# Performance work log

Measured on AMD Instinct MI355X. Metric: run time of the kernel, lower is better.

The kernel has to match this reference:

```python
import jax, jax.numpy as jnp
import numpy as np

N_NODES = 50000
K_CHEB = 3


def _norm_weights(edge_index, num_nodes):
    # PyG ChebConv with normalization='sym', lambda_max=2.0:
    # L_hat = (2/lambda_max) * (I - D^-1/2 A D^-1/2) - I = -D^-1/2 A D^-1/2
    src, dst = edge_index[0], edge_index[1]
    ones = jnp.ones(src.shape[0], dtype=jnp.float32)
    deg = jax.ops.segment_sum(ones, src, num_segments=num_nodes)
    dis = jnp.where(deg > 0, jax.lax.rsqrt(jnp.maximum(deg, 1.0)), 0.0)
    w = dis[src] * dis[dst]  # [E]
    return src, dst, w


def _cheb_conv(x, src, dst, w, W, b, num_nodes):
    # W: [K, in, out], b: [out]
    def lap(v):  # L_hat @ v = -(D^-1/2 A D^-1/2) v via gather + segment-sum
        return -jax.ops.segment_sum(w[:, None] * v[src], dst, num_segments=num_nodes)
    Tx0 = x
    out = Tx0 @ W[0]
    Tx1 = lap(x)
    out = out + Tx1 @ W[1]
    for k in range(2, W.shape[0]):
        Tx2 = 2.0 * lap(Tx1) - Tx0
        out = out + Tx2 @ W[k]
        Tx0, Tx1 = Tx1, Tx2
    return out + b


def setup_inputs() -> dict:
    key = jax.random.key(0)
    ks = jax.random.split(key, 9)
    N, E, F_IN, F_HID, F_OUT = N_NODES, 800000, 128, 64, 16
    x = jax.random.normal(ks[0], (N, F_IN), dtype=jnp.float32)
    edge_index = jax.random.randint(ks[1], (2, E), 0, N, dtype=jnp.int64)
    def glorot(k, kk, fi, fo):
        s = (6.0 / (fi + fo)) ** 0.5
        return jax.random.uniform(k, (kk, fi, fo), jnp.float32, -s, s)
    W1 = glorot(ks[2], K_CHEB, F_IN, F_HID)
    b1 = jnp.zeros((F_HID,), jnp.float32)
    Wm = glorot(ks[3], K_CHEB, F_HID, F_HID)
    bm = jnp.zeros((F_HID,), jnp.float32)
    W2 = glorot(ks[4], K_CHEB, F_HID, F_OUT)
    b2 = jnp.zeros((F_OUT,), jnp.float32)
    return {"x": x, "edge_index": edge_index, "W1": W1, "b1": b1,
            "Wm": Wm, "bm": bm, "W2": W2, "b2": b2}


def reference(x, edge_index, W1, b1, Wm, bm, W2, b2):
    src, dst, w = _norm_weights(edge_index, N_NODES)
    h = jax.nn.relu(_cheb_conv(x, src, dst, w, W1, b1, N_NODES))
    # dropout is identity in eval mode (training=False)
    h = jax.nn.relu(_cheb_conv(h, src, dst, w, Wm, bm, N_NODES))
    out = _cheb_conv(h, src, dst, w, W2, b2, N_NODES)
    return out
```

## Files before the change

kernel.cpp:

```cpp
#include <hip/hip_runtime.h>
#include <hip/hip_fp16.h>

constexpr int NNODES = 50000;
constexpr int NS  = 64;
constexpr int NR  = 4;
constexpr int RSZ = 12500;

typedef _Float16 half8_t __attribute__((ext_vector_type(8)));
typedef _Float16 half4_t __attribute__((ext_vector_type(4)));
typedef float    f32x4_t __attribute__((ext_vector_type(4)));

template<int CH> struct hvec_sel;
template<> struct hvec_sel<4> { using T = half4_t; };
template<> struct hvec_sel<8> { using T = half8_t; };


template<int FIN, int FOUT>
__device__ void pack_dev(const float* __restrict__ W, _Float16* __restrict__ Bp,
                         int b, int nb) {
  constexpr int NT = 3 * FOUT / 16;
  constexpr int KT = FIN / 32;
  const int total = KT * NT * 512;
  for (int i = b * 256 + (int)threadIdx.x; i < total; i += nb * 256) {
    int j = i & 7;
    int lane = (i >> 3) & 63;
    int tile = i >> 9;
    int nt = tile % NT, kt = tile / NT;
    int k = kt * 32 + (lane >> 4) * 8 + j;
    int n = nt * 16 + (lane & 15);
    int cheb = n / FOUT, c = n - cheb * FOUT;
    Bp[i] = (_Float16)W[((size_t)cheb * FIN + k) * FOUT + c];
  }
}

template<int FIN, int FOUT, typename IN_T>
__device__ void gemm_dev(const IN_T* __restrict__ X, const _Float16* __restrict__ Bp,
                         const float* __restrict__ b, _Float16* __restrict__ A,
                         _Float16* __restrict__ U, _Float16* __restrict__ V,
                         int N, int blk, _Float16* xs) {
  constexpr int NT = 3 * FOUT / 16;
  constexpr int C3 = NT / 3;
  constexpr int KT = FIN / 32;
  constexpr int LDR = FIN + 8;

  const int tid = threadIdx.x;
  const int row0 = blk * 64;

  for (int i = tid * 4; i < 64 * FIN; i += 1024) {
    int r = i / FIN, k = i - r * FIN;
    int row = row0 + r;
    short4 hv = make_short4(0, 0, 0, 0);
    if (row < N) {
      if constexpr (sizeof(IN_T) == 4) {
        float4 v = *(const float4*)((const float*)X + (size_t)row * FIN + k);
        _Float16 h0 = (_Float16)v.x, h1 = (_Float16)v.y, h2 = (_Float16)v.z, h3 = (_Float16)v.w;
        hv = make_short4(*(short*)&h0, *(short*)&h1, *(short*)&h2, *(short*)&h3);
      } else {
        hv = *(const short4*)((const _Float16*)X + (size_t)row * FIN + k);
      }
    }
    *(short4*)(&xs[r * LDR + k]) = hv;
  }
  __syncthreads();

  const int wave = tid >> 6, lane = tid & 63;
  const int m = lane & 15, quad = lane >> 4;

  f32x4_t acc[NT];
  #pragma unroll
  for (int nt = 0; nt < NT; ++nt) acc[nt] = (f32x4_t){0.f, 0.f, 0.f, 0.f};

  #pragma unroll
  for (int kt = 0; kt < KT; ++kt) {
    half8_t a = *(const half8_t*)(&xs[(wave * 16 + m) * LDR + kt * 32 + quad * 8]);
    const half8_t* bp = (const half8_t*)Bp + (size_t)(kt * NT) * 64 + lane;
    #pragma unroll
    for (int nt = 0; nt < NT; ++nt) {
      half8_t bf = bp[(size_t)nt * 64];
      acc[nt] = __builtin_amdgcn_mfma_f32_16x16x32_f16(a, bf, acc[nt], 0, 0, 0);
    }
  }

  const int row_b = row0 + wave * 16 + quad * 4;
  #pragma unroll
  for (int nt = 0; nt < C3; ++nt) {
    int c = nt * 16 + m;
    float bb = b[c];
    #pragma unroll
    for (int r = 0; r < 4; ++r) {
      int row = row_b + r;
      if (row < N) {
        size_t o = (size_t)row * FOUT + c;
        A[o] = (_Float16)(acc[nt][r] - acc[nt + 2 * C3][r] + bb);
        U[o] = (_Float16)acc[nt + C3][r];
        V[o] = (_Float16)acc[nt + 2 * C3][r];
      }
    }
  }
}


__global__ void __launch_bounds__(256) k1_hist_pack(const int* __restrict__ ei, int E, int ES,
    int* __restrict__ part_src, int* __restrict__ part_dst,
    const float* __restrict__ W1, const float* __restrict__ Wm, const float* __restrict__ W2,
    _Float16* __restrict__ Bp1, _Float16* __restrict__ Bp2, _Float16* __restrict__ Bp3) {
  __shared__ int sh[RSZ];
  const int bid = blockIdx.x;
  if (bid < 512) {
    const int z = bid & 1, r = (bid >> 1) & 3, s = bid >> 3;
    for (int i = threadIdx.x; i < RSZ; i += 256) sh[i] = 0;
    __syncthreads();
    const int lo = r * RSZ;
    const int* __restrict__ idxarr = ei + (z ? E : 0);
    const int e0 = s * ES, e1 = min(e0 + ES, E);
    for (int e = e0 + (int)threadIdx.x; e < e1; e += 256) {
      unsigned u = (unsigned)(idxarr[e] - lo);
      if (u < (unsigned)RSZ) atomicAdd(&sh[u], 1);
    }
    __syncthreads();
    int* __restrict__ part = z ? part_dst : part_src;
    const int base = (s * NR + r) * RSZ;
    for (int i = threadIdx.x; i < RSZ; i += 256) part[base + i] = sh[i];
  } else if (bid < 536) {
    pack_dev<128, 64>(W1, Bp1, bid - 512, 24);
  } else if (bid < 548) {
    pack_dev<64, 64>(Wm, Bp2, bid - 536, 12);
  } else {
    pack_dev<64, 16>(W2, Bp3, bid - 548, 3);
  }
}


__global__ void __launch_bounds__(256) k2_reduce_scan(const int* __restrict__ part_src,
    int* __restrict__ part_dst, float* __restrict__ dis, int* __restrict__ cnt,
    int* __restrict__ exc, int* __restrict__ bsum, int N) {
  __shared__ int sh[256];
  const int tid = threadIdx.x;
  const int n = blockIdx.x * 256 + tid;
  int off = 0;
  if (n < N) {
    int r = n / RSZ, i = n - r * RSZ;
    int ssum = 0;
    #pragma unroll 4
    for (int s = 0; s < NS; ++s) ssum += part_src[(size_t)(s * NR + r) * RSZ + i];
    dis[n] = (ssum > 0) ? rsqrtf((float)ssum) : 0.0f;
    for (int s = 0; s < NS; ++s) {
      size_t idx = (size_t)(s * NR + r) * RSZ + i;
      int c = part_dst[idx];
      part_dst[idx] = off;
      off += c;
    }
    cnt[n] = off;
  }
  int acc = off;
  sh[tid] = acc; __syncthreads();
  #pragma unroll
  for (int o = 1; o < 256; o <<= 1) {
    int t = (tid >= o) ? sh[tid - o] : 0;
    __syncthreads();
    acc += t;
    sh[tid] = acc;
    __syncthreads();
  }
  if (n < N) exc[n] = acc - off;
  if (tid == 255) bsum[blockIdx.x] = acc;
}


__global__ void __launch_bounds__(256) k2b_scan2(int* __restrict__ bsum, int NB) {
  __shared__ int sh[256];
  int tid = threadIdx.x;
  int v = (tid < NB) ? bsum[tid] : 0;
  int acc = v;
  sh[tid] = acc; __syncthreads();
  #pragma unroll
  for (int o = 1; o < 256; o <<= 1) {
    int t = (tid >= o) ? sh[tid - o] : 0;
    __syncthreads();
    acc += t;
    sh[tid] = acc;
    __syncthreads();
  }
  if (tid < NB) bsum[tid] = acc - v;
}


__global__ void __launch_bounds__(256) k3_fill_gemm1(const int* __restrict__ ei, int E, int ES,
    const int* __restrict__ exc, const int* __restrict__ bsumx,
    const int* __restrict__ pd_off, const float* __restrict__ dis, int2* __restrict__ ew,
    const float* __restrict__ x, const _Float16* __restrict__ Bp1, const float* __restrict__ b1,
    _Float16* __restrict__ Ah, _Float16* __restrict__ Uh, _Float16* __restrict__ Vh, int N) {
  __shared__ __align__(16) char smem[50048];
  const int bid = blockIdx.x;
  if (bid < 256) {
    int* cur = (int*)smem;
    for (int i = threadIdx.x; i < RSZ; i += 256) cur[i] = 0;
    __syncthreads();
    const int s = bid >> 2, r = bid & 3;
    const int lo = r * RSZ;
    const int base = (s * NR + r) * RSZ;
    const int e0 = s * ES, e1 = min(e0 + ES, E);
    for (int e = e0 + (int)threadIdx.x; e < e1; e += 256) {
      int sv = ei[e], d = ei[E + e];
      unsigned u = (unsigned)(d - lo);
      if (u < (unsigned)RSZ) {
        int rank = atomicAdd(&cur[u], 1);
        int pos = exc[d] + bsumx[d >> 8] + pd_off[base + u] + rank;
        float w = -dis[sv] * dis[d];
        ew[pos] = make_int2(sv, __float_as_int(w));
      }
    }
  } else {
    gemm_dev<128, 64, float>(x, Bp1, b1, Ah, Uh, Vh, N, bid - 256, (_Float16*)smem);
  }
}


template<int FIN, int FOUT>
__global__ void __launch_bounds__(256) gemm_mfma_kernel(const _Float16* __restrict__ X,
    const _Float16* __restrict__ Bp, const float* __restrict__ b,
    _Float16* __restrict__ A, _Float16* __restrict__ U, _Float16* __restrict__ V, int N) {
  __shared__ _Float16 xs[64 * (FIN + 8)];
  gemm_dev<FIN, FOUT, _Float16>(X, Bp, b, A, U, V, N, blockIdx.x, xs);
}


template<int F, int CH>
__global__ void __launch_bounds__(256) lapA_kernel(const void* __restrict__ Vp,
    const void* __restrict__ Up, void* __restrict__ Yp,
    const int* __restrict__ exc, const int* __restrict__ cnt, const int* __restrict__ bsumx,
    const int2* __restrict__ ew, int N) {
  using HT = typename hvec_sel<CH>::T;
  constexpr int H = F / CH;
  const HT* __restrict__ Vv = (const HT*)Vp;
  int t = blockIdx.x * 256 + threadIdx.x;
  int n = t / H;
  if (n >= N) return;
  int h = t - n * H;
  int j = exc[n] + bsumx[n >> 8];
  int e = j + cnt[n];
  float acc[CH];
  #pragma unroll
  for (int i = 0; i < CH; ++i) acc[i] = 0.f;
  for (; j + 7 < e; j += 8) {
    int2 c[8]; HT v[8];
    #pragma unroll
    for (int q = 0; q < 8; ++q) c[q] = ew[j + q];
    #pragma unroll
    for (int q = 0; q < 8; ++q) v[q] = Vv[(size_t)c[q].x * H + h];
    #pragma unroll
    for (int q = 0; q < 8; ++q) {
      float w = __int_as_float(c[q].y);
      #pragma unroll
      for (int i = 0; i < CH; ++i) acc[i] = fmaf(w, (float)v[q][i], acc[i]);
    }
  }
  for (; j + 3 < e; j += 4) {
    int2 c[4]; HT v[4];
    #pragma unroll
    for (int q = 0; q < 4; ++q) c[q] = ew[j + q];
    #pragma unroll
    for (int q = 0; q < 4; ++q) v[q] = Vv[(size_t)c[q].x * H + h];
    #pragma unroll
    for (int q = 0; q < 4; ++q) {
      float w = __int_as_float(c[q].y);
      #pragma unroll
      for (int i = 0; i < CH; ++i) acc[i] = fmaf(w, (float)v[q][i], acc[i]);
    }
  }
  for (; j < e; ++j) {
    int2 c = ew[j];
    float w = __int_as_float(c.y);
    HT v = Vv[(size_t)c.x * H + h];
    #pragma unroll
    for (int i = 0; i < CH; ++i) acc[i] = fmaf(w, (float)v[i], acc[i]);
  }
  HT u = ((const HT*)Up)[t];
  HT y;
  #pragma unroll
  for (int i = 0; i < CH; ++i) y[i] = (_Float16)fmaf(2.f, acc[i], (float)u[i]);
  ((HT*)Yp)[t] = y;
}

template<int F, int CH, bool RELU, bool OUT32>
__global__ void __launch_bounds__(256) lapB_kernel(const void* __restrict__ Yp,
    const void* __restrict__ Ap,
    const int* __restrict__ exc, const int* __restrict__ cnt, const int* __restrict__ bsumx,
    const int2* __restrict__ ew, void* __restrict__ outp, int N) {
  using HT = typename hvec_sel<CH>::T;
  constexpr int H = F / CH;
  const HT* __restrict__ Yv = (const HT*)Yp;
  int t = blockIdx.x * 256 + threadIdx.x;
  int n = t / H;
  if (n >= N) return;
  int h = t - n * H;
  int j = exc[n] + bsumx[n >> 8];
  int e = j + cnt[n];
  float acc[CH];
  #pragma unroll
  for (int i = 0; i < CH; ++i) acc[i] = 0.f;
  for (; j + 7 < e; j += 8) {
    int2 c[8]; HT v[8];
    #pragma unroll
    for (int q = 0; q < 8; ++q) c[q] = ew[j + q];
    #pragma unroll
    for (int q = 0; q < 8; ++q) v[q] = Yv[(size_t)c[q].x * H + h];
    #pragma unroll
    for (int q = 0; q < 8; ++q) {
      float w = __int_as_float(c[q].y);
      #pragma unroll
      for (int i = 0; i < CH; ++i) acc[i] = fmaf(w, (float)v[q][i], acc[i]);
    }
  }
  for (; j + 3 < e; j += 4) {
    int2 c[4]; HT v[4];
    #pragma unroll
    for (int q = 0; q < 4; ++q) c[q] = ew[j + q];
    #pragma unroll
    for (int q = 0; q < 4; ++q) v[q] = Yv[(size_t)c[q].x * H + h];
    #pragma unroll
    for (int q = 0; q < 4; ++q) {
      float w = __int_as_float(c[q].y);
      #pragma unroll
      for (int i = 0; i < CH; ++i) acc[i] = fmaf(w, (float)v[q][i], acc[i]);
    }
  }
  for (; j < e; ++j) {
    int2 c = ew[j];
    float w = __int_as_float(c.y);
    HT v = Yv[(size_t)c.x * H + h];
    #pragma unroll
    for (int i = 0; i < CH; ++i) acc[i] = fmaf(w, (float)v[i], acc[i]);
  }
  HT a = ((const HT*)Ap)[t];
  float r[CH];
  #pragma unroll
  for (int i = 0; i < CH; ++i) {
    r[i] = (float)a[i] + acc[i];
    if (RELU) r[i] = fmaxf(r[i], 0.f);
  }
  if constexpr (OUT32) {
    float4* o4 = (float4*)outp;
    #pragma unroll
    for (int q = 0; q < CH / 4; ++q)
      o4[(size_t)t * (CH / 4) + q] = make_float4(r[4 * q], r[4 * q + 1], r[4 * q + 2], r[4 * q + 3]);
  } else {
    HT y;
    #pragma unroll
    for (int i = 0; i < CH; ++i) y[i] = (_Float16)r[i];
    ((HT*)outp)[t] = y;
  }
}


extern "C" void kernel_launch(void* const* d_in, const int* in_sizes, int n_in,
                              void* d_out, int out_size, void* d_ws, size_t ws_size,
                              hipStream_t stream) {
  const float* x  = (const float*)d_in[0];
  const int*   ei = (const int*)d_in[1];
  const float* W1 = (const float*)d_in[2];
  const float* b1 = (const float*)d_in[3];
  const float* Wm = (const float*)d_in[4];
  const float* bm = (const float*)d_in[5];
  const float* W2 = (const float*)d_in[6];
  const float* b2 = (const float*)d_in[7];
  float* out = (float*)d_out;
  const int N = NNODES;
  const int E = in_sizes[1] / 2;
  const int ES = (E + NS - 1) / NS;
  const int NB = (N + 255) / 256;

  char* p = (char*)d_ws;
  auto alloc = [&](size_t bytes) -> char* {
    char* q = p;
    p += (bytes + 255) & ~(size_t)255;
    return q;
  };
  int*      part_src = (int*)alloc((size_t)NS * NR * RSZ * 4);
  int*      part_dst = (int*)alloc((size_t)NS * NR * RSZ * 4);
  int*      cnt      = (int*)alloc((size_t)N * 4);
  int*      exc      = (int*)alloc((size_t)N * 4);
  int*      bsum     = (int*)alloc(1024);
  float*    dis      = (float*)alloc((size_t)N * 4);
  int2*     ew       = (int2*)alloc((size_t)E * 8);
  _Float16* Xh       = (_Float16*)alloc((size_t)N * 64 * 2);
  _Float16* Ah       = (_Float16*)alloc((size_t)N * 64 * 2);
  _Float16* Uh       = (_Float16*)alloc((size_t)N * 64 * 2);
  _Float16* Vh       = (_Float16*)alloc((size_t)N * 64 * 2);
  _Float16* Yh       = (_Float16*)alloc((size_t)N * 64 * 2);
  _Float16* Bp1      = (_Float16*)alloc((size_t)128 * 192 * 2);
  _Float16* Bp2      = (_Float16*)alloc((size_t)64 * 192 * 2);
  _Float16* Bp3      = (_Float16*)alloc((size_t)64 * 48 * 2);

  k1_hist_pack<<<551, 256, 0, stream>>>(ei, E, ES, part_src, part_dst,
                                        W1, Wm, W2, Bp1, Bp2, Bp3);
  k2_reduce_scan<<<NB, 256, 0, stream>>>(part_src, part_dst, dis, cnt, exc, bsum, N);
  k2b_scan2<<<1, 256, 0, stream>>>(bsum, NB);
  k3_fill_gemm1<<<256 + 782, 256, 0, stream>>>(ei, E, ES, exc, bsum, part_dst, dis, ew,
                                               x, Bp1, b1, Ah, Uh, Vh, N);

  const int gmm  = (N + 63) / 64;
  const int g64c = (N * 8 + 255) / 256;
  const int g16c = (N * 4 + 255) / 256;

  lapA_kernel<64, 8><<<g64c, 256, 0, stream>>>(Vh, Uh, Yh, exc, cnt, bsum, ew, N);
  lapB_kernel<64, 8, true, false><<<g64c, 256, 0, stream>>>(Yh, Ah, exc, cnt, bsum, ew, Xh, N);

  gemm_mfma_kernel<64, 64><<<gmm, 256, 0, stream>>>(Xh, Bp2, bm, Ah, Uh, Vh, N);
  lapA_kernel<64, 8><<<g64c, 256, 0, stream>>>(Vh, Uh, Yh, exc, cnt, bsum, ew, N);
  lapB_kernel<64, 8, true, false><<<g64c, 256, 0, stream>>>(Yh, Ah, exc, cnt, bsum, ew, Xh, N);

  gemm_mfma_kernel<64, 16><<<gmm, 256, 0, stream>>>(Xh, Bp3, b2, Ah, Uh, Vh, N);
  lapA_kernel<16, 4><<<g16c, 256, 0, stream>>>(Vh, Uh, Yh, exc, cnt, bsum, ew, N);
  lapB_kernel<16, 4, false, true><<<g16c, 256, 0, stream>>>(Yh, Ah, exc, cnt, bsum, ew, out, N);
}
```

Measured before the change: 269.4 us.

## Compress edge list to 32-bit packed src+fp16 weight and factor dst scaling

Packs each CSR edge into 32 bits: a 16-bit source index and the fp16 source-side normalisation. The destination-side dis factor moves out of the per-edge weight and is applied once per node in the Laplacian epilogues. Histogram partials shrink to u16 with an s*N layout, and per-edge ranks are recorded during the histogram so the fill pass no longer needs shared-memory atomics. The aim is to cut edge-stream bandwidth in all six SpMM passes and the cost of the preprocessing. In exchange it relies on N < 65536 and per-slice degree < 256, and lowers weight precision to fp16.

```diff
diff --git a/kernel.cpp b/kernel.cpp
--- a/kernel.cpp
+++ b/kernel.cpp
@@ -13,6 +13,11 @@
 template<int CH> struct hvec_sel;
 template<> struct hvec_sel<4> { using T = half4_t; };
 template<> struct hvec_sel<8> { using T = half8_t; };
+
+__device__ __forceinline__ float w_of(unsigned ec) {
+  unsigned short wb = (unsigned short)(ec >> 16);
+  return (float)__builtin_bit_cast(_Float16, wb);
+}
 
 
 template<int FIN, int FOUT>
@@ -101,9 +106,11 @@
 
 
 __global__ void __launch_bounds__(256) k1_hist_pack(const int* __restrict__ ei, int E, int ES,
-    int* __restrict__ part_src, int* __restrict__ part_dst,
+    unsigned short* __restrict__ part_src, unsigned short* __restrict__ part_dst,
+    unsigned char* __restrict__ rank,
     const float* __restrict__ W1, const float* __restrict__ Wm, const float* __restrict__ W2,
-    _Float16* __restrict__ Bp1, _Float16* __restrict__ Bp2, _Float16* __restrict__ Bp3) {
+    _Float16* __restrict__ Bp1, _Float16* __restrict__ Bp2, _Float16* __restrict__ Bp3,
+    int N) {
   __shared__ int sh[RSZ];
   const int bid = blockIdx.x;
   if (bid < 512) {
@@ -113,14 +120,25 @@
     const int lo = r * RSZ;
     const int* __restrict__ idxarr = ei + (z ? E : 0);
     const int e0 = s * ES, e1 = min(e0 + ES, E);
-    for (int e = e0 + (int)threadIdx.x; e < e1; e += 256) {
-      unsigned u = (unsigned)(idxarr[e] - lo);
-      if (u < (unsigned)RSZ) atomicAdd(&sh[u], 1);
-    }
-    __syncthreads();
-    int* __restrict__ part = z ? part_dst : part_src;
-    const int base = (s * NR + r) * RSZ;
-    for (int i = threadIdx.x; i < RSZ; i += 256) part[base + i] = sh[i];
+    if (z) {
+      for (int e = e0 + (int)threadIdx.x; e < e1; e += 256) {
+        unsigned u = (unsigned)(idxarr[e] - lo);
+        if (u < (unsigned)RSZ) {
+          int rk = atomicAdd(&sh[u], 1);
+          rank[e] = (unsigned char)rk;
+        }
+      }
+    } else {
+      for (int e = e0 + (int)threadIdx.x; e < e1; e += 256) {
+        unsigned u = (unsigned)(idxarr[e] - lo);
+        if (u < (unsigned)RSZ) atomicAdd(&sh[u], 1);
+      }
+    }
+    __syncthreads();
+    unsigned short* __restrict__ part = z ? part_dst : part_src;
+    const size_t base = (size_t)s * N + lo;
+    for (int i = threadIdx.x; i < RSZ && lo + i < N; i += 256)
+      part[base + i] = (unsigned short)sh[i];
   } else if (bid < 536) {
     pack_dev<128, 64>(W1, Bp1, bid - 512, 24);
   } else if (bid < 548) {
@@ -131,23 +149,22 @@
 }
 
 
-__global__ void __launch_bounds__(256) k2_reduce_scan(const int* __restrict__ part_src,
-    int* __restrict__ part_dst, float* __restrict__ dis, int* __restrict__ cnt,
+__global__ void __launch_bounds__(256) k2_reduce_scan(const unsigned short* __restrict__ part_src,
+    unsigned short* __restrict__ part_dst, _Float16* __restrict__ dis, int* __restrict__ cnt,
     int* __restrict__ exc, int* __restrict__ bsum, int N) {
   __shared__ int sh[256];
   const int tid = threadIdx.x;
   const int n = blockIdx.x * 256 + tid;
   int off = 0;
   if (n < N) {
-    int r = n / RSZ, i = n - r * RSZ;
     int ssum = 0;
     #pragma unroll 4
-    for (int s = 0; s < NS; ++s) ssum += part_src[(size_t)(s * NR + r) * RSZ + i];
-    dis[n] = (ssum > 0) ? rsqrtf((float)ssum) : 0.0f;
+    for (int s = 0; s < NS; ++s) ssum += part_src[(size_t)s * N + n];
+    dis[n] = (_Float16)((ssum > 0) ? rsqrtf((float)ssum) : 0.0f);
     for (int s = 0; s < NS; ++s) {
-      size_t idx = (size_t)(s * NR + r) * RSZ + i;
+      size_t idx = (size_t)s * N + n;
       int c = part_dst[idx];
-      part_dst[idx] = off;
+      part_dst[idx] = (unsigned short)off;
       off += c;
     }
     cnt[n] = off;
@@ -187,31 +204,22 @@
 
 __global__ void __launch_bounds__(256) k3_fill_gemm1(const int* __restrict__ ei, int E, int ES,
     const int* __restrict__ exc, const int* __restrict__ bsumx,
-    const int* __restrict__ pd_off, const float* __restrict__ dis, int2* __restrict__ ew,
+    const unsigned short* __restrict__ pd_off, const unsigned char* __restrict__ rank,
+    const unsigned short* __restrict__ dis_u, unsigned* __restrict__ ew,
     const float* __restrict__ x, const _Float16* __restrict__ Bp1, const float* __restrict__ b1,
     _Float16* __restrict__ Ah, _Float16* __restrict__ Uh, _Float16* __restrict__ Vh, int N) {
-  __shared__ __align__(16) char smem[50048];
+  __shared__ _Float16 xs[64 * (128 + 8)];
   const int bid = blockIdx.x;
   if (bid < 256) {
-    int* cur = (int*)smem;
-    for (int i = threadIdx.x; i < RSZ; i += 256) cur[i] = 0;
-    __syncthreads();
-    const int s = bid >> 2, r = bid & 3;
-    const int lo = r * RSZ;
-    const int base = (s * NR + r) * RSZ;
-    const int e0 = s * ES, e1 = min(e0 + ES, E);
-    for (int e = e0 + (int)threadIdx.x; e < e1; e += 256) {
+    for (int e = bid * 256 + (int)threadIdx.x; e < E; e += 256 * 256) {
       int sv = ei[e], d = ei[E + e];
-      unsigned u = (unsigned)(d - lo);
-      if (u < (unsigned)RSZ) {
-        int rank = atomicAdd(&cur[u], 1);
-        int pos = exc[d] + bsumx[d >> 8] + pd_off[base + u] + rank;
-        float w = -dis[sv] * dis[d];
-        ew[pos] = make_int2(sv, __float_as_int(w));
-      }
+      int s = e / ES;
+      int pos = exc[d] + bsumx[d >> 8] + (int)pd_off[(size_t)s * N + d] + (int)rank[e];
+      unsigned w16 = dis_u[sv];
+      ew[pos] = (unsigned)sv | (w16 << 16);
     }
   } else {
-    gemm_dev<128, 64, float>(x, Bp1, b1, Ah, Uh, Vh, N, bid - 256, (_Float16*)smem);
+    gemm_dev<128, 64, float>(x, Bp1, b1, Ah, Uh, Vh, N, bid - 256, xs);
   }
 }
 
@@ -229,7 +237,7 @@
 __global__ void __launch_bounds__(256) lapA_kernel(const void* __restrict__ Vp,
     const void* __restrict__ Up, void* __restrict__ Yp,
     const int* __restrict__ exc, const int* __restrict__ cnt, const int* __restrict__ bsumx,
-    const int2* __restrict__ ew, int N) {
+    const unsigned* __restrict__ ew, const _Float16* __restrict__ dis, int N) {
   using HT = typename hvec_sel<CH>::T;
   constexpr int H = F / CH;
   const HT* __restrict__ Vv = (const HT*)Vp;
@@ -243,42 +251,43 @@
   #pragma unroll
   for (int i = 0; i < CH; ++i) acc[i] = 0.f;
   for (; j + 7 < e; j += 8) {
-    int2 c[8]; HT v[8];
+    unsigned c[8]; HT v[8];
     #pragma unroll
     for (int q = 0; q < 8; ++q) c[q] = ew[j + q];
     #pragma unroll
-    for (int q = 0; q < 8; ++q) v[q] = Vv[(size_t)c[q].x * H + h];
+    for (int q = 0; q < 8; ++q) v[q] = Vv[(size_t)(c[q] & 0xFFFF) * H + h];
     #pragma unroll
     for (int q = 0; q < 8; ++q) {
-      float w = __int_as_float(c[q].y);
+      float w = w_of(c[q]);
       #pragma unroll
       for (int i = 0; i < CH; ++i) acc[i] = fmaf(w, (float)v[q][i], acc[i]);
     }
   }
   for (; j + 3 < e; j += 4) {
-    int2 c[4]; HT v[4];
+    unsigned c[4]; HT v[4];
     #pragma unroll
     for (int q = 0; q < 4; ++q) c[q] = ew[j + q];
     #pragma unroll
-    for (int q = 0; q < 4; ++q) v[q] = Vv[(size_t)c[q].x * H + h];
+    for (int q = 0; q < 4; ++q) v[q] = Vv[(size_t)(c[q] & 0xFFFF) * H + h];
     #pragma unroll
     for (int q = 0; q < 4; ++q) {
-      float w = __int_as_float(c[q].y);
+      float w = w_of(c[q]);
       #pragma unroll
       for (int i = 0; i < CH; ++i) acc[i] = fmaf(w, (float)v[q][i], acc[i]);
     }
   }
   for (; j < e; ++j) {
-    int2 c = ew[j];
-    float w = __int_as_float(c.y);
-    HT v = Vv[(size_t)c.x * H + h];
+    unsigned c = ew[j];
+    float w = w_of(c);
+    HT v = Vv[(size_t)(c & 0xFFFF) * H + h];
     #pragma unroll
     for (int i = 0; i < CH; ++i) acc[i] = fmaf(w, (float)v[i], acc[i]);
   }
+  float s2 = -2.f * (float)dis[n];
   HT u = ((const HT*)Up)[t];
   HT y;
   #pragma unroll
-  for (int i = 0; i < CH; ++i) y[i] = (_Float16)fmaf(2.f, acc[i], (float)u[i]);
+  for (int i = 0; i < CH; ++i) y[i] = (_Float16)fmaf(s2, acc[i], (float)u[i]);
   ((HT*)Yp)[t] = y;
 }
 
@@ -286,7 +295,8 @@
 __global__ void __launch_bounds__(256) lapB_kernel(const void* __restrict__ Yp,
     const void* __restrict__ Ap,
     const int* __restrict__ exc, const int* __restrict__ cnt, const int* __restrict__ bsumx,
-    const int2* __restrict__ ew, void* __restrict__ outp, int N) {
+    const unsigned* __restrict__ ew, const _Float16* __restrict__ dis,
+    void* __restrict__ outp, int N) {
   using HT = typename hvec_sel<CH>::T;
   constexpr int H = F / CH;
   const HT* __restrict__ Yv = (const HT*)Yp;
@@ -300,43 +310,44 @@
   #pragma unroll
   for (int i = 0; i < CH; ++i) acc[i] = 0.f;
   for (; j + 7 < e; j += 8) {
-    int2 c[8]; HT v[8];
+    unsigned c[8]; HT v[8];
     #pragma unroll
     for (int q = 0; q < 8; ++q) c[q] = ew[j + q];
     #pragma unroll
-    for (int q = 0; q < 8; ++q) v[q] = Yv[(size_t)c[q].x * H + h];
+    for (int q = 0; q < 8; ++q) v[q] = Yv[(size_t)(c[q] & 0xFFFF) * H + h];
     #pragma unroll
     for (int q = 0; q < 8; ++q) {
-      float w = __int_as_float(c[q].y);
+      float w = w_of(c[q]);
       #pragma unroll
       for (int i = 0; i < CH; ++i) acc[i] = fmaf(w, (float)v[q][i], acc[i]);
     }
   }
   for (; j + 3 < e; j += 4) {
-    int2 c[4]; HT v[4];
+    unsigned c[4]; HT v[4];
     #pragma unroll
     for (int q = 0; q < 4; ++q) c[q] = ew[j + q];
     #pragma unroll
-    for (int q = 0; q < 4; ++q) v[q] = Yv[(size_t)c[q].x * H + h];
+    for (int q = 0; q < 4; ++q) v[q] = Yv[(size_t)(c[q] & 0xFFFF) * H + h];
     #pragma unroll
     for (int q = 0; q < 4; ++q) {
-      float w = __int_as_float(c[q].y);
+      float w = w_of(c[q]);
       #pragma unroll
       for (int i = 0; i < CH; ++i) acc[i] = fmaf(w, (float)v[q][i], acc[i]);
     }
   }
   for (; j < e; ++j) {
-    int2 c = ew[j];
-    float w = __int_as_float(c.y);
-    HT v = Yv[(size_t)c.x * H + h];
+    unsigned c = ew[j];
+    float w = w_of(c);
+    HT v = Yv[(size_t)(c & 0xFFFF) * H + h];
     #pragma unroll
     for (int i = 0; i < CH; ++i) acc[i] = fmaf(w, (float)v[i], acc[i]);
   }
+  float s1 = -(float)dis[n];
   HT a = ((const HT*)Ap)[t];
   float r[CH];
   #pragma unroll
   for (int i = 0; i < CH; ++i) {
-    r[i] = (float)a[i] + acc[i];
+    r[i] = fmaf(s1, acc[i], (float)a[i]);
     if (RELU) r[i] = fmaxf(r[i], 0.f);
   }
   if constexpr (OUT32) {
@@ -376,41 +387,43 @@
     p += (bytes + 255) & ~(size_t)255;
     return q;
   };
-  int*      part_src = (int*)alloc((size_t)NS * NR * RSZ * 4);
-  int*      part_dst = (int*)alloc((size_t)NS * NR * RSZ * 4);
-  int*      cnt      = (int*)alloc((size_t)N * 4);
-  int*      exc      = (int*)alloc((size_t)N * 4);
-  int*      bsum     = (int*)alloc(1024);
-  float*    dis      = (float*)alloc((size_t)N * 4);
-  int2*     ew       = (int2*)alloc((size_t)E * 8);
-  _Float16* Xh       = (_Float16*)alloc((size_t)N * 64 * 2);
-  _Float16* Ah       = (_Float16*)alloc((size_t)N * 64 * 2);
-  _Float16* Uh       = (_Float16*)alloc((size_t)N * 64 * 2);
-  _Float16* Vh       = (_Float16*)alloc((size_t)N * 64 * 2);
-  _Float16* Yh       = (_Float16*)alloc((size_t)N * 64 * 2);
-  _Float16* Bp1      = (_Float16*)alloc((size_t)128 * 192 * 2);
-  _Float16* Bp2      = (_Float16*)alloc((size_t)64 * 192 * 2);
-  _Float16* Bp3      = (_Float16*)alloc((size_t)64 * 48 * 2);
-
-  k1_hist_pack<<<551, 256, 0, stream>>>(ei, E, ES, part_src, part_dst,
-                                        W1, Wm, W2, Bp1, Bp2, Bp3);
+  unsigned short* part_src = (unsigned short*)alloc((size_t)NS * N * 2);
+  unsigned short* part_dst = (unsigned short*)alloc((size_t)NS * N * 2);
+  unsigned char*  rank     = (unsigned char*)alloc((size_t)E);
+  int*            cnt      = (int*)alloc((size_t)N * 4);
+  int*            exc      = (int*)alloc((size_t)N * 4);
+  int*            bsum     = (int*)alloc(1024);
+  _Float16*       dis      = (_Float16*)alloc((size_t)N * 2);
+  unsigned*       ew       = (unsigned*)alloc((size_t)E * 4);
+  _Float16* Xh  = (_Float16*)alloc((size_t)N * 64 * 2);
+  _Float16* Ah  = (_Float16*)alloc((size_t)N * 64 * 2);
+  _Float16* Uh  = (_Float16*)alloc((size_t)N * 64 * 2);
+  _Float16* Vh  = (_Float16*)alloc((size_t)N * 64 * 2);
+  _Float16* Yh  = (_Float16*)alloc((size_t)N * 64 * 2);
+  _Float16* Bp1 = (_Float16*)alloc((size_t)128 * 192 * 2);
+  _Float16* Bp2 = (_Float16*)alloc((size_t)64 * 192 * 2);
+  _Float16* Bp3 = (_Float16*)alloc((size_t)64 * 48 * 2);
+
+  k1_hist_pack<<<551, 256, 0, stream>>>(ei, E, ES, part_src, part_dst, rank,
+                                        W1, Wm, W2, Bp1, Bp2, Bp3, N);
   k2_reduce_scan<<<NB, 256, 0, stream>>>(part_src, part_dst, dis, cnt, exc, bsum, N);
   k2b_scan2<<<1, 256, 0, stream>>>(bsum, NB);
-  k3_fill_gemm1<<<256 + 782, 256, 0, stream>>>(ei, E, ES, exc, bsum, part_dst, dis, ew,
+  k3_fill_gemm1<<<256 + 782, 256, 0, stream>>>(ei, E, ES, exc, bsum, part_dst, rank,
+                                               (const unsigned short*)dis, ew,
                                                x, Bp1, b1, Ah, Uh, Vh, N);
 
   const int gmm  = (N + 63) / 64;
   const int g64c = (N * 8 + 255) / 256;
   const int g16c = (N * 4 + 255) / 256;
 
-  lapA_kernel<64, 8><<<g64c, 256, 0, stream>>>(Vh, Uh, Yh, exc, cnt, bsum, ew, N);
-  lapB_kernel<64, 8, true, false><<<g64c, 256, 0, stream>>>(Yh, Ah, exc, cnt, bsum, ew, Xh, N);
+  lapA_kernel<64, 8><<<g64c, 256, 0, stream>>>(Vh, Uh, Yh, exc, cnt, bsum, ew, dis, N);
+  lapB_kernel<64, 8, true, false><<<g64c, 256, 0, stream>>>(Yh, Ah, exc, cnt, bsum, ew, dis, Xh, N);
 
   gemm_mfma_kernel<64, 64><<<gmm, 256, 0, stream>>>(Xh, Bp2, bm, Ah, Uh, Vh, N);
-  lapA_kernel<64, 8><<<g64c, 256, 0, stream>>>(Vh, Uh, Yh, exc, cnt, bsum, ew, N);
-  lapB_kernel<64, 8, true, false><<<g64c, 256, 0, stream>>>(Yh, Ah, exc, cnt, bsum, ew, Xh, N);
+  lapA_kernel<64, 8><<<g64c, 256, 0, stream>>>(Vh, Uh, Yh, exc, cnt, bsum, ew, dis, N);
+  lapB_kernel<64, 8, true, false><<<g64c, 256, 0, stream>>>(Yh, Ah, exc, cnt, bsum, ew, dis, Xh, N);
 
   gemm_mfma_kernel<64, 16><<<gmm, 256, 0, stream>>>(Xh, Bp3, b2, Ah, Uh, Vh, N);
-  lapA_kernel<16, 4><<<g16c, 256, 0, stream>>>(Vh, Uh, Yh, exc, cnt, bsum, ew, N);
-  lapB_kernel<16, 4, false, true><<<g16c, 256, 0, stream>>>(Yh, Ah, exc, cnt, bsum, ew, out, N);
-}
+  lapA_kernel<16, 4><<<g16c, 256, 0, stream>>>(Vh, Uh, Yh, exc, cnt, bsum, ew, dis, N);
+  lapB_kernel<16, 4, false, true><<<g16c, 256, 0, stream>>>(Yh, Ah, exc, cnt, bsum, ew, dis, out, N);
+}
```

After: 250.4 us. 1.08x faster.
